# Kernel optimization log

Measured on AMD Instinct MI355X. Metric: run time of the kernel, lower is better.

Reference implementation:

```python
import jax, jax.numpy as jnp
import numpy as np

ALPHA = 0.2      # LeakyReLU negative slope
NEG = -9e15     # mask fill value, as in pyGAT

B, N, NFEAT, NHID, NCLASS, NHEADS = 4, 2048, 128, 64, 32, 8


def setup_inputs() -> dict:
    key = jax.random.key(0)
    ks = jax.random.split(key, 8)
    x = jax.random.normal(ks[0], (B, N, NFEAT), dtype=jnp.float32)
    adj = jax.random.randint(ks[1], (B, N, N), 0, 2, dtype=jnp.int32)
    W = jax.random.normal(ks[2], (NHEADS, NFEAT, NHID), dtype=jnp.float32) * 0.1
    a1 = jax.random.normal(ks[3], (NHEADS, NHID), dtype=jnp.float32) * 0.1
    a2 = jax.random.normal(ks[4], (NHEADS, NHID), dtype=jnp.float32) * 0.1
    Wo = jax.random.normal(ks[5], (NHEADS * NHID, NCLASS), dtype=jnp.float32) * 0.1
    ao1 = jax.random.normal(ks[6], (NCLASS,), dtype=jnp.float32) * 0.1
    ao2 = jax.random.normal(ks[7], (NCLASS,), dtype=jnp.float32) * 0.1
    return {"x": x, "adj": adj, "W": W, "a1": a1, "a2": a2,
            "Wo": Wo, "ao1": ao1, "ao2": ao2}


def _gat_forward(x, adj, W, a1, a2, Wo, ao1, ao2):
    mask = adj > 0  # [B, N, N]
    # --- multi-head layer (concat=True) ---
    Wh = jnp.einsum('bnf,hfd->bhnd', x, W)          # [B,H,N,nhid]
    f1 = jnp.einsum('bhnd,hd->bhn', Wh, a1)          # Wh @ a[:nhid]
    f2 = jnp.einsum('bhnd,hd->bhn', Wh, a2)          # Wh @ a[nhid:]
    e = jax.nn.leaky_relu(f1[..., :, None] + f2[..., None, :], ALPHA)
    att = jax.nn.softmax(jnp.where(mask[:, None], e, NEG), axis=-1)
    h = jax.nn.elu(jnp.einsum('bhnm,bhmd->bhnd', att, Wh))  # [B,H,N,nhid]
    # torch.cat along dim=2: [B, N, H*nhid]
    h = jnp.transpose(h, (0, 2, 1, 3)).reshape(B, N, NHEADS * NHID)
    # (dropout layers are no-ops in eval mode)
    # --- output head (concat=False, no ELU) ---
    Wh2 = jnp.einsum('bnf,fc->bnc', h, Wo)           # [B,N,nclass]
    g1 = jnp.einsum('bnc,c->bn', Wh2, ao1)
    g2 = jnp.einsum('bnc,c->bn', Wh2, ao2)
    e2 = jax.nn.leaky_relu(g1[:, :, None] + g2[:, None, :], ALPHA)
    att2 = jax.nn.softmax(jnp.where(mask, e2, NEG), axis=-1)
    return jnp.einsum('bnm,bmc->bnc', att2, Wh2)     # [B,N,nclass]


def reference(x, adj, W, a1, a2, Wo, ao1, ao2):
    return _gat_forward(x, adj, W, a1, a2, Wo, ao1, ao2)
```

## Files before the change

### kernel.cpp

```cpp
#include <hip/hip_runtime.h>


typedef _Float16 half8  __attribute__((ext_vector_type(8)));
typedef _Float16 half2_ __attribute__((ext_vector_type(2)));
typedef float  float4_ __attribute__((ext_vector_type(4)));
typedef unsigned int uint4_ __attribute__((ext_vector_type(4)));

#if __has_builtin(__builtin_amdgcn_exp2f)
#define EXP2(x) __builtin_amdgcn_exp2f(x)
#else
#define EXP2(x) __expf((x) * 0.69314718055994531f)
#endif
#define LOG2E 1.44269504088896340f

static __device__ __forceinline__ unsigned pkh(float a, float b) {
#if __has_builtin(__builtin_amdgcn_cvt_pkrtz)
  return __builtin_bit_cast(unsigned, __builtin_amdgcn_cvt_pkrtz(a, b));
#else
  half2_ h = {(_Float16)a, (_Float16)b};
  return __builtin_bit_cast(unsigned, h);
#endif
}
static __device__ __forceinline__ unsigned short f2h(float f) {
  _Float16 h = (_Float16)f;
  return __builtin_bit_cast(unsigned short, h);
}

static __device__ __forceinline__ unsigned bitm(unsigned mb, int jj) {
#if __has_builtin(__builtin_amdgcn_sbfe)
  return (unsigned)__builtin_amdgcn_sbfe((int)mb, jj, 1);
#else
  return 0u - ((mb >> jj) & 1u);
#endif
}
static __device__ __forceinline__ unsigned pmask(unsigned s0, unsigned s1) {
  return __builtin_amdgcn_perm(s1, s0, 0x05040100u);
}
static __device__ __forceinline__ unsigned wmaxh(unsigned u, unsigned u2,
    unsigned pm, half2_ Ah, half2_ A2h) {
  half2_ p = Ah * __builtin_bit_cast(half2_, u);
  half2_ n = A2h * __builtin_bit_cast(half2_, u2);
  half2_ m = __builtin_elementwise_max(p, n);
  return __builtin_bit_cast(unsigned, m) & pm;
}

__global__ __launch_bounds__(256) void k_wfrag(
    const float* __restrict__ Wm, const float* __restrict__ Wo,
    unsigned short* __restrict__ Wf, unsigned short* __restrict__ WoF) {
  if (blockIdx.x < 32) {
    const int T = blockIdx.x * 256 + threadIdx.x;
    const int lane = T & 63;
    int r = T >> 6;
    const int nt = r & 3; r >>= 2;
    const int kstep = r & 3; r >>= 2;
    const int h = r;
    const int kk = kstep * 32 + (lane >> 4) * 8;
    const int n = nt * 16 + (lane & 15);
    const float* sp = Wm + h * 8192 + kk * 64 + n;
    unsigned short o[8];
    #pragma unroll
    for (int jj = 0; jj < 8; ++jj) o[jj] = f2h(sp[jj * 64]);
    *(uint4_*)(Wf + T * 8) = *(uint4_*)o;
  } else {
    const int T = (blockIdx.x - 32) * 256 + threadIdx.x;
    const int lane = T & 63;
    const int nt = (T >> 6) & 1, kstep = T >> 7;
    const int kk = kstep * 32 + (lane >> 4) * 8;
    const int n = nt * 16 + (lane & 15);
    unsigned short o[8];
    #pragma unroll
    for (int jj = 0; jj < 8; ++jj) o[jj] = f2h(Wo[(kk + jj) * 32 + n]);
    *(uint4_*)(WoF + T * 8) = *(uint4_*)o;
  }
}

__global__ __launch_bounds__(256) void k_front(
    const int* __restrict__ adj, unsigned long long* __restrict__ maskb,
    const float* __restrict__ x, const unsigned short* __restrict__ Wf,
    const float* __restrict__ a1, const float* __restrict__ a2,
    unsigned short* __restrict__ WhF, float* __restrict__ f1,
    unsigned short* __restrict__ Uv, unsigned short* __restrict__ U2v) {
  __shared__ float wsm[64 * 68];
  const int bx = blockIdx.x;
  const int t = threadIdx.x;
  if (bx >= 1024) {
    const int lane = t & 63, wid = t >> 6;
    const int s = lane & 15;
    const long long row0 = (long long)(bx - 1024) * 4;
    for (int rr = 0; rr < 4; ++rr) {
      const long long row = row0 + rr;
      const int4* src = (const int4*)(adj + row * 2048);
      #pragma unroll
      for (int c = 0; c < 2; ++c) {
        int4 v = src[c * 256 + t];
        unsigned nib = (v.x != 0 ? 1u : 0u) | (v.y != 0 ? 2u : 0u) |
                       (v.z != 0 ? 4u : 0u) | (v.w != 0 ? 8u : 0u);
        unsigned lo = (s < 8) ? (nib << (s * 4)) : 0u;
        unsigned hi = (s >= 8) ? (nib << ((s - 8) * 4)) : 0u;
        #pragma unroll
        for (int off = 1; off < 16; off <<= 1) {
          lo |= __shfl_xor(lo, off);
          hi |= __shfl_xor(hi, off);
        }
        if (s == 0) {
          int word = c * 16 + wid * 4 + (lane >> 4);
          maskb[row * 32 + word] = ((unsigned long long)hi << 32) | (unsigned long long)lo;
        }
      }
    }
    return;
  }
  const int itile = bx & 31, bh = bx >> 5;
  const int b = bh >> 3, h = bh & 7;
  const int i0 = itile * 64;
  const int lane = t & 63, w = t >> 6;
  const int cl = lane & 15, q = lane >> 4;
  const float* xrow = x + ((long long)b * 2048 + i0 + w * 16 + cl) * 128;
  const unsigned short* wfh = Wf + h * 8192;
  float4_ acc0 = {0.f, 0.f, 0.f, 0.f}, acc1 = acc0, acc2 = acc0, acc3 = acc0;
  #pragma unroll
  for (int kstep = 0; kstep < 4; ++kstep) {
    const float* xp = xrow + kstep * 32 + q * 8;
    const float4 xa = *(const float4*)xp;
    const float4 xb = *(const float4*)(xp + 4);
    uint4_ ap;
    ap.x = pkh(xa.x, xa.y);
    ap.y = pkh(xa.z, xa.w);
    ap.z = pkh(xb.x, xb.y);
    ap.w = pkh(xb.z, xb.w);
    const half8 af = __builtin_bit_cast(half8, ap);
    const unsigned short* bp = wfh + kstep * 2048 + lane * 8;
    const half8 b0 = *(const half8*)(bp);
    const half8 b1 = *(const half8*)(bp + 512);
    const half8 b2 = *(const half8*)(bp + 1024);
    const half8 b3 = *(const half8*)(bp + 1536);
    acc0 = __builtin_amdgcn_mfma_f32_16x16x32_f16(af, b0, acc0, 0, 0, 0);
    acc1 = __builtin_amdgcn_mfma_f32_16x16x32_f16(af, b1, acc1, 0, 0, 0);
    acc2 = __builtin_amdgcn_mfma_f32_16x16x32_f16(af, b2, acc2, 0, 0, 0);
    acc3 = __builtin_amdgcn_mfma_f32_16x16x32_f16(af, b3, acc3, 0, 0, 0);
  }
  {
    float4_ accs[4] = {acc0, acc1, acc2, acc3};
    #pragma unroll
    for (int nt = 0; nt < 4; ++nt)
      #pragma unroll
      for (int reg = 0; reg < 4; ++reg)
        wsm[(w * 16 + q * 4 + reg) * 68 + nt * 16 + cl] = accs[nt][reg];
  }
  __syncthreads();
  {
    const int row = t >> 2, seg = t & 3;
    const float* wr = wsm + row * 68 + seg * 16;
    const float4* a1p = (const float4*)(a1 + h * 64 + seg * 16);
    const float4* a2p = (const float4*)(a2 + h * 64 + seg * 16);
    float p1 = 0.f, p2 = 0.f;
    #pragma unroll
    for (int u = 0; u < 4; ++u) {
      const float4 wv = *(const float4*)(wr + u * 4);
      const float4 v1 = a1p[u];
      const float4 v2 = a2p[u];
      p1 += wv.x * v1.x + wv.y * v1.y + wv.z * v1.z + wv.w * v1.w;
      p2 += wv.x * v2.x + wv.y * v2.y + wv.z * v2.z + wv.w * v2.w;
    }
    p1 += __shfl_xor(p1, 1); p1 += __shfl_xor(p1, 2);
    p2 += __shfl_xor(p2, 1); p2 += __shfl_xor(p2, 2);
    if (seg == 0) {
      f1[(long long)bh * 2048 + i0 + row] = p1 * LOG2E;
      const float s2 = p2 * LOG2E;
      Uv[(long long)bh * 2048 + i0 + row] = f2h(EXP2(s2));
      U2v[(long long)bh * 2048 + i0 + row] = f2h(EXP2(0.2f * s2));
    }
  }
  #pragma unroll
  for (int u = 0; u < 2; ++u) {
    const int idx = u * 256 + t;
    const int l2 = idx & 63, nt2 = (idx >> 6) & 3, ks2 = idx >> 8;
    const int jrow = ks2 * 32 + (l2 >> 4) * 8;
    const int d = nt2 * 16 + (l2 & 15);
    uint4_ o;
    o.x = pkh(wsm[(jrow + 0) * 68 + d], wsm[(jrow + 1) * 68 + d]);
    o.y = pkh(wsm[(jrow + 2) * 68 + d], wsm[(jrow + 3) * 68 + d]);
    o.z = pkh(wsm[(jrow + 4) * 68 + d], wsm[(jrow + 5) * 68 + d]);
    o.w = pkh(wsm[(jrow + 6) * 68 + d], wsm[(jrow + 7) * 68 + d]);
    const long long off = (long long)bh * 131072 + (long long)itile * 4096 +
                          ks2 * 2048 + nt2 * 512 + l2 * 8;
    *(uint4_*)(WhF + off) = o;
  }
}

__global__ __launch_bounds__(256) void k_attn1(
    const unsigned short* __restrict__ whf, const float* __restrict__ f1v,
    const unsigned short* __restrict__ Uv, const unsigned short* __restrict__ U2v,
    const unsigned long long* __restrict__ maskb, unsigned short* __restrict__ hA) {
  __shared__ unsigned short bsm[2][8192];
  __shared__ unsigned short Us[2048], U2s[2048];
  const int bh = blockIdx.y, b = bh >> 3, hh = bh & 7;
  const int t = threadIdx.x;
  const int lane = t & 63, wid = t >> 6;
  const int cl = lane & 15, q = lane >> 4;
  const long long i_g = (long long)blockIdx.x * 64 + wid * 16 + cl;
  const float f1i = f1v[(long long)bh * 2048 + i_g];
  const float A = EXP2(f1i), A2 = EXP2(0.2f * f1i);
  const half2_ Ah = __builtin_bit_cast(half2_, pkh(A, A));
  const half2_ A2h = __builtin_bit_cast(half2_, pkh(A2, A2));
  const uint2* mpp = (const uint2*)(maskb + ((long long)b * 2048 + i_g) * 32);
  const unsigned short* whfb = whf + (long long)bh * 131072;
  const float4* gB = (const float4*)whfb;
  const half8 vones = {1.0f16, 1.0f16, 1.0f16, 1.0f16, 1.0f16, 1.0f16, 1.0f16, 1.0f16};
  ((uint4_*)Us)[t]  = ((const uint4_*)(Uv  + (long long)bh * 2048))[t];
  ((uint4_*)U2s)[t] = ((const uint4_*)(U2v + (long long)bh * 2048))[t];
  {
    float4 st0[4];
    #pragma unroll
    for (int u = 0; u < 4; ++u) st0[u] = gB[u * 256 + t];
    #pragma unroll
    for (int u = 0; u < 4; ++u) ((float4*)bsm[0])[u * 256 + t] = st0[u];
  }
  uint2 mw0_c = mpp[0], mw1_c = mpp[1];
  float4_ acc0 = {0.f, 0.f, 0.f, 0.f}, acc1 = acc0, acc2 = acc0, acc3 = acc0;
  float4_ accz = acc0;
  const int qs = q * 8;
  for (int s = 0; s < 16; ++s) {
    float4 stn0, stn1, stn2, stn3;
    if (s < 15) {
      const float4* gp = gB + (s + 1) * 1024 + t;
      stn0 = gp[0]; stn1 = gp[256]; stn2 = gp[512]; stn3 = gp[768];
    }
    const uint2 mwA = mw0_c, mwB = mw1_c;
    if (s < 15) { mw0_c = mpp[s * 2 + 2]; mw1_c = mpp[s * 2 + 3]; }
    __syncthreads();
    const unsigned short* bsb = bsm[s & 1] + lane * 8;
    #pragma unroll
    for (int jc2 = 0; jc2 < 2; ++jc2) {
      const int jc = s * 2 + jc2;
      const uint2 mw = jc2 ? mwB : mwA;
      #pragma unroll
      for (int ks = 0; ks < 2; ++ks) {
        const unsigned mb = (ks ? mw.y : mw.x) >> qs;
        const uint4_ uv  = *(const uint4_*)(Us  + jc * 64 + ks * 32 + qs);
        const uint4_ u2v = *(const uint4_*)(U2s + jc * 64 + ks * 32 + qs);
        const unsigned s0 = bitm(mb, 0), s1 = bitm(mb, 1), s2 = bitm(mb, 2),
                       s3 = bitm(mb, 3), s4 = bitm(mb, 4), s5 = bitm(mb, 5),
                       s6 = bitm(mb, 6), s7 = bitm(mb, 7);
        uint4_ pk;
        pk.x = wmaxh(uv.x, u2v.x, pmask(s0, s1), Ah, A2h);
        pk.y = wmaxh(uv.y, u2v.y, pmask(s2, s3), Ah, A2h);
        pk.z = wmaxh(uv.z, u2v.z, pmask(s4, s5), Ah, A2h);
        pk.w = wmaxh(uv.w, u2v.w, pmask(s6, s7), Ah, A2h);
        const half8 af = __builtin_bit_cast(half8, pk);
        const unsigned short* bp = bsb + (jc2 * 2 + ks) * 2048;
        const half8 b0 = *(const half8*)(bp);
        const half8 b1 = *(const half8*)(bp + 512);
        const half8 b2 = *(const half8*)(bp + 1024);
        const half8 b3 = *(const half8*)(bp + 1536);
        acc0 = __builtin_amdgcn_mfma_f32_16x16x32_f16(af, b0, acc0, 0, 0, 0);
        acc1 = __builtin_amdgcn_mfma_f32_16x16x32_f16(af, b1, acc1, 0, 0, 0);
        acc2 = __builtin_amdgcn_mfma_f32_16x16x32_f16(af, b2, acc2, 0, 0, 0);
        acc3 = __builtin_amdgcn_mfma_f32_16x16x32_f16(af, b3, acc3, 0, 0, 0);
        accz = __builtin_amdgcn_mfma_f32_16x16x32_f16(af, vones, accz, 0, 0, 0);
      }
    }
    if (s < 15) {
      float4* dp = (float4*)bsm[(s + 1) & 1] + t;
      dp[0] = stn0; dp[256] = stn1; dp[512] = stn2; dp[768] = stn3;
    }
  }
  __syncthreads();
  float* hs = (float*)bsm;
  {
    float4_ accs[4] = {acc0, acc1, acc2, acc3};
    #pragma unroll
    for (int reg = 0; reg < 4; ++reg) {
      const float rz = 1.f / accz[reg];
      #pragma unroll
      for (int nt = 0; nt < 4; ++nt) {
        float v = accs[nt][reg] * rz;
        v = (v > 0.f) ? v : (__expf(v) - 1.f);
        hs[(wid * 16 + q * 4 + reg) * 68 + nt * 16 + cl] = v;
      }
    }
  }
  __syncthreads();
  const int rtg0 = b * 128 + blockIdx.x * 4;
  #pragma unroll
  for (int u = 0; u < 2; ++u) {
    const int id = u * 256 + t;
    const int l2 = id & 63, ks2 = (id >> 6) & 1, rtile = id >> 7;
    const int rowl = rtile * 16 + (l2 & 15);
    const int d = ks2 * 32 + (l2 >> 4) * 8;
    const float* hp = hs + rowl * 68 + d;
    uint4_ o;
    o.x = pkh(hp[0], hp[1]); o.y = pkh(hp[2], hp[3]);
    o.z = pkh(hp[4], hp[5]); o.w = pkh(hp[6], hp[7]);
    const long long rt = rtg0 + rtile;
    const int kstep = hh * 2 + ks2;
    *(uint4_*)(hA + ((rt * 16 + kstep) * 64 + l2) * 8) = o;
  }
}

__global__ __launch_bounds__(128) void k_ogemm(
    const unsigned short* __restrict__ hA, const unsigned short* __restrict__ WoF,
    const float* __restrict__ ao1, const float* __restrict__ ao2,
    unsigned short* __restrict__ Wh2F, float* __restrict__ g1,
    unsigned short* __restrict__ gU, unsigned short* __restrict__ gU2) {
  __shared__ float w2s[32 * 36];
  const int t = threadIdx.x, lane = t & 63, wv = t >> 6;
  const int cl = lane & 15, q = lane >> 4;
  const long long rt = (long long)blockIdx.x * 2 + wv;
  float4_ acc0 = {0.f, 0.f, 0.f, 0.f}, acc1 = acc0;
  const unsigned short* ap = hA + rt * 8192 + lane * 8;
  const unsigned short* bp = WoF + lane * 8;
  #pragma unroll
  for (int kstep = 0; kstep < 16; ++kstep) {
    const half8 af = *(const half8*)(ap + kstep * 512);
    const half8 b0 = *(const half8*)(bp + kstep * 1024);
    const half8 b1 = *(const half8*)(bp + kstep * 1024 + 512);
    acc0 = __builtin_amdgcn_mfma_f32_16x16x32_f16(af, b0, acc0, 0, 0, 0);
    acc1 = __builtin_amdgcn_mfma_f32_16x16x32_f16(af, b1, acc1, 0, 0, 0);
  }
  const float o1a = ao1[cl], o1b = ao1[cl + 16];
  const float o2a = ao2[cl], o2b = ao2[cl + 16];
  #pragma unroll
  for (int reg = 0; reg < 4; ++reg) {
    const int rowl = wv * 16 + q * 4 + reg;
    w2s[rowl * 36 + cl] = acc0[reg];
    w2s[rowl * 36 + 16 + cl] = acc1[reg];
    float p1 = acc0[reg] * o1a + acc1[reg] * o1b;
    float p2 = acc0[reg] * o2a + acc1[reg] * o2b;
    p1 += __shfl_xor(p1, 1); p1 += __shfl_xor(p1, 2);
    p1 += __shfl_xor(p1, 4); p1 += __shfl_xor(p1, 8);
    p2 += __shfl_xor(p2, 1); p2 += __shfl_xor(p2, 2);
    p2 += __shfl_xor(p2, 4); p2 += __shfl_xor(p2, 8);
    if (cl == 0) {
      const long long row = (long long)blockIdx.x * 32 + rowl;
      g1[row] = p1 * LOG2E;
      const float s2 = p2 * LOG2E;
      gU[row]  = f2h(EXP2(s2));
      gU2[row] = f2h(EXP2(0.2f * s2));
    }
  }
  __syncthreads();
  {
    const int l2 = t & 63, nt2 = t >> 6;
    const int g = blockIdx.x >> 6, jc = (blockIdx.x >> 1) & 31, ks2 = blockIdx.x & 1;
    const int kb = (l2 >> 4) * 8, n = nt2 * 16 + (l2 & 15);
    uint4_ o;
    o.x = pkh(w2s[(kb + 0) * 36 + n], w2s[(kb + 1) * 36 + n]);
    o.y = pkh(w2s[(kb + 2) * 36 + n], w2s[(kb + 3) * 36 + n]);
    o.z = pkh(w2s[(kb + 4) * 36 + n], w2s[(kb + 5) * 36 + n]);
    o.w = pkh(w2s[(kb + 6) * 36 + n], w2s[(kb + 7) * 36 + n]);
    const long long off = (long long)g * 65536 + jc * 2048 + ks2 * 1024 +
                          nt2 * 512 + l2 * 8;
    *(uint4_*)(Wh2F + off) = o;
  }
}

__global__ __launch_bounds__(256) void k_attn2(
    const unsigned short* __restrict__ whf2, const float* __restrict__ g1v,
    const unsigned short* __restrict__ gU, const unsigned short* __restrict__ gU2,
    const unsigned long long* __restrict__ maskb, float* __restrict__ outp) {
  __shared__ float accs[4][16][33];
  __shared__ float zsh[64];
  const int b = blockIdx.y;
  const long long i0 = (long long)blockIdx.x * 16;
  const int t = threadIdx.x, lane = t & 63, wid = t >> 6;
  const int cl = lane & 15, q = lane >> 4;
  const float g1i = g1v[(long long)b * 2048 + i0 + cl];
  const float A = EXP2(g1i), A2 = EXP2(0.2f * g1i);
  const half2_ Ah = __builtin_bit_cast(half2_, pkh(A, A));
  const half2_ A2h = __builtin_bit_cast(half2_, pkh(A2, A2));
  const uint2* mpp = (const uint2*)(maskb + ((long long)b * 2048 + i0 + cl) * 32);
  const unsigned short* ub = gU + (long long)b * 2048;
  const unsigned short* u2b = gU2 + (long long)b * 2048;
  const unsigned short* wb = whf2 + (long long)b * 65536;
  const half8 vones = {1.0f16, 1.0f16, 1.0f16, 1.0f16, 1.0f16, 1.0f16, 1.0f16, 1.0f16};
  float4_ acc0 = {0.f, 0.f, 0.f, 0.f}, acc1 = acc0, accz = acc0;
  const int qs = q * 8;
  const int jc0 = wid * 8;
  uint2 mw_c = mpp[jc0];
  uint4_ ua_c  = *(const uint4_*)(ub  + jc0 * 64 + qs);
  uint4_ u2a_c = *(const uint4_*)(u2b + jc0 * 64 + qs);
  uint4_ ubn_c  = *(const uint4_*)(ub  + jc0 * 64 + 32 + qs);
  uint4_ u2b_c = *(const uint4_*)(u2b + jc0 * 64 + 32 + qs);
  for (int c8 = 0; c8 < 8; ++c8) {
    const int jc = jc0 + c8;
    const uint2 mw = mw_c;
    const uint4_ uA = ua_c, u2A = u2a_c, uB = ubn_c, u2B = u2b_c;
    {
      const int jn = jc + ((c8 < 7) ? 1 : 0);
      mw_c = mpp[jn];
      ua_c  = *(const uint4_*)(ub  + jn * 64 + qs);
      u2a_c = *(const uint4_*)(u2b + jn * 64 + qs);
      ubn_c  = *(const uint4_*)(ub  + jn * 64 + 32 + qs);
      u2b_c = *(const uint4_*)(u2b + jn * 64 + 32 + qs);
    }
    const unsigned short* bb = wb + (jc * 2) * 1024 + lane * 8;
    #pragma unroll
    for (int ks = 0; ks < 2; ++ks) {
      const unsigned mb = (ks ? mw.y : mw.x) >> qs;
      const uint4_ uv  = ks ? uB : uA;
      const uint4_ u2v = ks ? u2B : u2A;
      const unsigned s0 = bitm(mb, 0), s1 = bitm(mb, 1), s2 = bitm(mb, 2),
                     s3 = bitm(mb, 3), s4 = bitm(mb, 4), s5 = bitm(mb, 5),
                     s6 = bitm(mb, 6), s7 = bitm(mb, 7);
      uint4_ pk;
      pk.x = wmaxh(uv.x, u2v.x, pmask(s0, s1), Ah, A2h);
      pk.y = wmaxh(uv.y, u2v.y, pmask(s2, s3), Ah, A2h);
      pk.z = wmaxh(uv.z, u2v.z, pmask(s4, s5), Ah, A2h);
      pk.w = wmaxh(uv.w, u2v.w, pmask(s6, s7), Ah, A2h);
      const half8 af = __builtin_bit_cast(half8, pk);
      const unsigned short* bk = bb + ks * 1024;
      const half8 b0 = *(const half8*)bk;
      const half8 b1 = *(const half8*)(bk + 512);
      acc0 = __builtin_amdgcn_mfma_f32_16x16x32_f16(af, b0, acc0, 0, 0, 0);
      acc1 = __builtin_amdgcn_mfma_f32_16x16x32_f16(af, b1, acc1, 0, 0, 0);
      accz = __builtin_amdgcn_mfma_f32_16x16x32_f16(af, vones, accz, 0, 0, 0);
    }
  }
  if (cl == 0) {
    #pragma unroll
    for (int reg = 0; reg < 4; ++reg) zsh[wid * 16 + q * 4 + reg] = accz[reg];
  }
  float4_ a01[2] = {acc0, acc1};
  #pragma unroll
  for (int nt = 0; nt < 2; ++nt)
    #pragma unroll
    for (int reg = 0; reg < 4; ++reg)
      accs[wid][q * 4 + reg][nt * 16 + cl] = a01[nt][reg];
  __syncthreads();
  #pragma unroll
  for (int r = 0; r < 2; ++r) {
    int o = r * 256 + t;
    int il = o >> 5, c = o & 31;
    float s = accs[0][il][c] + accs[1][il][c] + accs[2][il][c] + accs[3][il][c];
    float Z = zsh[il] + zsh[16 + il] + zsh[32 + il] + zsh[48 + il];
    outp[((long long)b * 2048 + i0 + il) * 32 + c] = s / Z;
  }
}

extern "C" void kernel_launch(void* const* d_in, const int* in_sizes, int n_in,
                              void* d_out, int out_size, void* d_ws, size_t ws_size,
                              hipStream_t stream) {
  const float* x   = (const float*)d_in[0];
  const int*   adj = (const int*)d_in[1];
  const float* W   = (const float*)d_in[2];
  const float* a1  = (const float*)d_in[3];
  const float* a2  = (const float*)d_in[4];
  const float* Wo  = (const float*)d_in[5];
  const float* ao1 = (const float*)d_in[6];
  const float* ao2 = (const float*)d_in[7];
  float* out = (float*)d_out;
  char* ws = (char*)d_ws;

  unsigned long long* maskb = (unsigned long long*)(ws + 0);
  unsigned short* Wf   = (unsigned short*)(ws + 2097152);
  unsigned short* WoF  = (unsigned short*)(ws + 2228224);
  unsigned short* WhF  = (unsigned short*)(ws + 18874368);
  float* f1   = (float*)(ws + 27262976);
  unsigned short* Uv  = (unsigned short*)(ws + 27525120);
  unsigned short* U2v = (unsigned short*)(ws + 27656192);
  unsigned short* hA  = (unsigned short*)(ws + 27787264);
  unsigned short* Wh2F = (unsigned short*)(ws + 45613056);
  float* g1   = (float*)(ws + 46137344);
  unsigned short* gU  = (unsigned short*)(ws + 46170112);
  unsigned short* gU2 = (unsigned short*)(ws + 46186496);

  hipLaunchKernelGGL(k_wfrag, dim3(40), dim3(256), 0, stream, W, Wo, Wf, WoF);
  hipLaunchKernelGGL(k_front, dim3(3072), dim3(256), 0, stream, adj, maskb,
                     x, Wf, a1, a2, WhF, f1, Uv, U2v);
  hipLaunchKernelGGL(k_attn1, dim3(32, 32), dim3(256), 0, stream, WhF, f1, Uv, U2v,
                     maskb, hA);
  hipLaunchKernelGGL(k_ogemm, dim3(256), dim3(128), 0, stream, hA, WoF, ao1, ao2,
                     Wh2F, g1, gU, gU2);
  hipLaunchKernelGGL(k_attn2, dim3(128, 4), dim3(256), 0, stream, Wh2F, g1, gU, gU2,
                     maskb, out);
}
```

Baseline: 165.9 us.

## Stage B tiles with direct global-to-LDS loads and stream one slice via registers

Replaces the register-staged double buffering of the Wh tile with global_load_lds transfers issued by three of the four waves, which removes the VGPR round trip and the separate LDS store phase. The fourth 16-column slice of each k-step is no longer placed in LDS at all. Each lane loads it straight from global memory into registers one iteration ahead. The barrier now sits at the top of the loop, before the next transfer is issued. Risks include relying on the compiler to insert the vmcnt waits needed for the asynchronous LDS writes, and a prefetch on the final iteration that reads one slice past the current head's data.

Measured after the change: 167.6 us. No clear change (+1.1%).

```diff
diff --git a/kernel.cpp b/kernel.cpp
--- a/kernel.cpp
+++ b/kernel.cpp
@@ -12,6 +12,14 @@
 #define EXP2(x) __expf((x) * 0.69314718055994531f)
 #endif
 #define LOG2E 1.44269504088896340f
+
+#if __has_builtin(__builtin_amdgcn_global_load_lds)
+#define GLDS(g, l) __builtin_amdgcn_global_load_lds( \
+    (const __attribute__((address_space(1))) unsigned*)(unsigned long long)(const void*)(g), \
+    (__attribute__((address_space(3))) unsigned*)(unsigned long long)(const void*)(l), 16, 0, 0)
+#else
+#define GLDS(g, l) (*(float4*)(void*)(l) = *(const float4*)(const void*)(g))
+#endif
 
 static __device__ __forceinline__ unsigned pkh(float a, float b) {
 #if __has_builtin(__builtin_amdgcn_cvt_pkrtz)
@@ -209,26 +217,31 @@
   const half8 vones = {1.0f16, 1.0f16, 1.0f16, 1.0f16, 1.0f16, 1.0f16, 1.0f16, 1.0f16};
   ((uint4_*)Us)[t]  = ((const uint4_*)(Uv  + (long long)bh * 2048))[t];
   ((uint4_*)U2s)[t] = ((const uint4_*)(U2v + (long long)bh * 2048))[t];
-  {
-    float4 st0[4];
-    #pragma unroll
-    for (int u = 0; u < 4; ++u) st0[u] = gB[u * 256 + t];
-    #pragma unroll
-    for (int u = 0; u < 4; ++u) ((float4*)bsm[0])[u * 256 + t] = st0[u];
+  if (wid < 3) {
+    const float4* gp = gB + t;
+    unsigned short* lp = bsm[0] + t * 8;
+    GLDS(gp,       lp);
+    GLDS(gp + 256, lp + 256 * 8);
+    GLDS(gp + 512, lp + 512 * 8);
+    GLDS(gp + 768, lp + 768 * 8);
   }
   uint2 mw0_c = mpp[0], mw1_c = mpp[1];
+  half8 b3_c = *(const half8*)(whfb + 1536 + lane * 8);
   float4_ acc0 = {0.f, 0.f, 0.f, 0.f}, acc1 = acc0, acc2 = acc0, acc3 = acc0;
   float4_ accz = acc0;
   const int qs = q * 8;
   for (int s = 0; s < 16; ++s) {
-    float4 stn0, stn1, stn2, stn3;
-    if (s < 15) {
+    __syncthreads();
+    if (s < 15 && wid < 3) {
       const float4* gp = gB + (s + 1) * 1024 + t;
-      stn0 = gp[0]; stn1 = gp[256]; stn2 = gp[512]; stn3 = gp[768];
+      unsigned short* lp = bsm[(s + 1) & 1] + t * 8;
+      GLDS(gp,       lp);
+      GLDS(gp + 256, lp + 256 * 8);
+      GLDS(gp + 512, lp + 512 * 8);
+      GLDS(gp + 768, lp + 768 * 8);
     }
     const uint2 mwA = mw0_c, mwB = mw1_c;
     if (s < 15) { mw0_c = mpp[s * 2 + 2]; mw1_c = mpp[s * 2 + 3]; }
-    __syncthreads();
     const unsigned short* bsb = bsm[s & 1] + lane * 8;
     #pragma unroll
     for (int jc2 = 0; jc2 < 2; ++jc2) {
@@ -236,6 +249,9 @@
       const uint2 mw = jc2 ? mwB : mwA;
       #pragma unroll
       for (int ks = 0; ks < 2; ++ks) {
+        const int it = s * 4 + jc2 * 2 + ks;
+        const half8 b3 = b3_c;
+        b3_c = *(const half8*)(whfb + (it + 1) * 2048 + 1536 + lane * 8);
         const unsigned mb = (ks ? mw.y : mw.x) >> qs;
         const uint4_ uv  = *(const uint4_*)(Us  + jc * 64 + ks * 32 + qs);
         const uint4_ u2v = *(const uint4_*)(U2s + jc * 64 + ks * 32 + qs);
@@ -252,17 +268,12 @@
         const half8 b0 = *(const half8*)(bp);
         const half8 b1 = *(const half8*)(bp + 512);
         const half8 b2 = *(const half8*)(bp + 1024);
-        const half8 b3 = *(const half8*)(bp + 1536);
         acc0 = __builtin_amdgcn_mfma_f32_16x16x32_f16(af, b0, acc0, 0, 0, 0);
         acc1 = __builtin_amdgcn_mfma_f32_16x16x32_f16(af, b1, acc1, 0, 0, 0);
         acc2 = __builtin_amdgcn_mfma_f32_16x16x32_f16(af, b2, acc2, 0, 0, 0);
         acc3 = __builtin_amdgcn_mfma_f32_16x16x32_f16(af, b3, acc3, 0, 0, 0);
         accz = __builtin_amdgcn_mfma_f32_16x16x32_f16(af, vones, accz, 0, 0, 0);
       }
-    }
-    if (s < 15) {
-      float4* dp = (float4*)bsm[(s + 1) & 1] + t;
-      dp[0] = stn0; dp[256] = stn1; dp[512] = stn2; dp[768] = stn3;
     }
   }
   __syncthreads();
```
